# Kernel optimization log

Hardware: AMD Instinct MI355X
Metric: run time of the kernel (lower is better)

The kernel has to match this reference:

```python
import jax, jax.numpy as jnp
import numpy as np

B, T = 64, 64
H = 256
CLIP = 0.2


def _conv(x, W, b, s):
    y = jax.lax.conv_general_dilated(x, W, (s, s), 'VALID',
                                     dimension_numbers=('NHWC', 'HWIO', 'NHWC'))
    return jax.nn.leaky_relu(y + b, negative_slope=0.2)


def _lstm(x, Wk, Wr, b):
    # keras LSTM, gate order i,f,g,o; x: (B,T,256) -> (B,T,256)
    h0 = jnp.zeros((x.shape[0], H), x.dtype)

    def step(carry, xt):
        h, c = carry
        z = xt @ Wk + h @ Wr + b
        i, f, g, o = jnp.split(z, 4, axis=-1)
        c = jax.nn.sigmoid(f) * c + jax.nn.sigmoid(i) * jnp.tanh(g)
        h = jax.nn.sigmoid(o) * jnp.tanh(c)
        return (h, c), h

    _, hs = jax.lax.scan(step, (h0, h0), jnp.swapaxes(x, 0, 1))
    return jnp.swapaxes(hs, 0, 1)


def setup_inputs():
    key = jax.random.key(0)
    ks = jax.random.split(key, 24)
    s = 0.05
    x = jax.random.normal(ks[0], (B, T, 13, 8, 8), jnp.float32)
    a_taken = jax.random.randint(ks[1], (B, T), 0, 36)
    mask = jax.random.randint(ks[2], (B, T, 4096), 0, 2).astype(jnp.int32)
    # taken actions must be legal (mask=1), as in real rollouts
    bi = jnp.repeat(jnp.arange(B), T)
    ti = jnp.tile(jnp.arange(T), B)
    mask = mask.at[bi, ti, a_taken.reshape(-1)].set(1)
    lg_prob_old = -jnp.abs(jax.random.normal(ks[3], (B, T), jnp.float32)) - 1.0
    GAE = jax.random.normal(ks[4], (B, T), jnp.float32)
    old_v_pred = jax.random.normal(ks[5], (B, T), jnp.float32)
    returns = jax.random.normal(ks[6], (B, T), jnp.float32)
    return {
        'x': x, 'mask': mask, 'lg_prob_old': lg_prob_old, 'a_taken': a_taken,
        'GAE': GAE, 'old_v_pred': old_v_pred, 'returns': returns,
        'W1': jax.random.normal(ks[7], (2, 2, 8, 16), jnp.float32) * s,
        'b1': jnp.zeros((16,), jnp.float32),
        'W2': jax.random.normal(ks[8], (2, 2, 16, 32), jnp.float32) * s,
        'b2': jnp.zeros((32,), jnp.float32),
        'W3': jax.random.normal(ks[9], (2, 2, 32, 64), jnp.float32) * s,
        'b3': jnp.zeros((64,), jnp.float32),
        'W4': jax.random.normal(ks[10], (1, 1, 64, 128), jnp.float32) * s,
        'b4': jnp.zeros((128,), jnp.float32),
        'lstm_k': jax.random.normal(ks[11], (256, 1024), jnp.float32) * s,
        'lstm_r': jax.random.normal(ks[12], (256, 1024), jnp.float32) * s,
        'lstm_b': jnp.zeros((1024,), jnp.float32),
        'pir_W': jax.random.normal(ks[13], (256, 36), jnp.float32) * s,
        'pir_b': jnp.zeros((36,), jnp.float32),
        'pim_W': jax.random.normal(ks[14], (256, 4096), jnp.float32) * s,
        'pim_b': jnp.zeros((4096,), jnp.float32),
        'v_W': jax.random.normal(ks[15], (256, 1), jnp.float32) * s,
        'v_b': jnp.zeros((1,), jnp.float32),
    }


def reference(x, mask, lg_prob_old, a_taken, GAE, old_v_pred, returns,
              W1, b1, W2, b2, W3, b3, W4, b4,
              lstm_k, lstm_r, lstm_b, pir_W, pir_b, pim_W, pim_b, v_W, v_b):
    Bn, Tn = x.shape[0], x.shape[1]
    h = x.reshape(Bn * Tn, 13, 8, 8)  # NHWC: H=13, W=8, C=8
    h = _conv(h, W1, b1, 2)  # (BT,6,4,16)
    h = _conv(h, W2, b2, 1)  # (BT,5,3,32)
    h = _conv(h, W3, b3, 2)  # (BT,2,1,64)
    h = _conv(h, W4, b4, 1)  # (BT,2,1,128)
    # keras Flatten(data_format='channels_first') permutes dim1 to last then flattens
    h = jnp.transpose(h, (0, 2, 3, 1)).reshape(Bn, Tn, -1)  # (B,T,256)
    lstm = _lstm(h, lstm_k, lstm_r, lstm_b).reshape(-1, H)  # (BT,256)

    pir = jax.nn.softmax(lstm @ pir_W + pir_b, axis=-1)  # (BT,36)
    maskf = mask.reshape(-1, 4096).astype(jnp.float32)
    pim = jax.nn.softmax(lstm @ pim_W + pim_b, axis=-1) * maskf
    scale = jnp.sum(pim, axis=1, keepdims=True)
    pim = pim / jnp.where(scale > 0, scale, jnp.ones_like(scale))  # (BT,4096)
    vpred = lstm @ v_W + v_b  # (BT,1)

    lg_old = lg_prob_old.reshape(-1)
    a = a_taken.reshape(-1)
    gae = GAE.reshape(-1)
    ovp = old_v_pred.reshape(-1)
    ret = returns.reshape(-1)
    gae = (gae - jnp.mean(gae)) / (jnp.std(gae) + 1e-8)

    t = jnp.arange(a.shape[0])
    p = jnp.where(t % 2 == 0, pir[t, a], pim[t, a])  # alternating heads
    lg_new = jnp.log(p)
    rt = jnp.exp(lg_new - lg_old)
    pg1 = -gae * rt
    pg2 = -gae * jnp.clip(rt, 1.0 - CLIP, 1.0 + CLIP)
    pg_loss = jnp.mean(jnp.maximum(pg1, pg2))

    # faithful to original TF: (BT,1) vpred broadcast against (BT,) -> (BT,BT)
    vpredclipped = ovp + jnp.clip(vpred - ovp, -CLIP, CLIP)
    vf1 = jnp.square(vpred - ret)
    vf2 = jnp.square(vpredclipped - ret)
    vf_loss = 0.5 * jnp.mean(jnp.maximum(vf1, vf2))

    pim_e = pim + (1.0 - maskf)
    entropy = -jnp.sum(pir * jnp.log(pir)) - jnp.sum(pim_e * jnp.log(pim_e))
    loss = pg_loss - entropy + vf_loss
    return (loss, pg_loss, entropy, vf_loss)
```

## Files before the change

### kernel.cpp

```cpp
#include <hip/hip_runtime.h>

typedef unsigned short u16;
typedef unsigned int   u32;

#define BT   4096
#define TSEQ 64
#define NB   64

typedef __attribute__((ext_vector_type(8))) short  short8;
typedef __attribute__((ext_vector_type(4))) float  f32x4;
typedef __attribute__((ext_vector_type(2))) _Float16 h2;

__device__ __forceinline__ float bf(u16 v) {
    u32 u = ((u32)v) << 16;
    return __builtin_bit_cast(float, u);
}
__device__ __forceinline__ u16 f2b(float f) {
    u32 u = __builtin_bit_cast(u32, f);
    return (u16)((u + 0x7fffu + ((u >> 16) & 1u)) >> 16);
}
__device__ __forceinline__ float lrelu(float x) { return x > 0.f ? x : 0.2f * x; }
__device__ __forceinline__ h2 i2h(int v) { return __builtin_bit_cast(h2, v); }
__device__ __forceinline__ float dot2(int hbits, int wbits, float acc) {
#if __has_builtin(__builtin_amdgcn_fdot2)
    return __builtin_amdgcn_fdot2(i2h(hbits), i2h(wbits), acc, false);
#else
    h2 a = i2h(hbits), b = i2h(wbits);
    return acc + (float)a.x * (float)b.x + (float)a.y * (float)b.y;
#endif
}
__device__ __forceinline__ float fsigm(float x) { return 1.f / (1.f + __expf(-x)); }
__device__ __forceinline__ float ftanh(float x) { return 1.f - 2.f / (__expf(2.f * x) + 1.f); }
__device__ __forceinline__ float ldf(const void* p, int i, int f32) {
    return f32 ? ((const float*)p)[i] : bf(((const u16*)p)[i]);
}
__device__ __forceinline__ u16 ldb(const void* p, int i, int f32) {
    return f32 ? f2b(((const float*)p)[i]) : ((const u16*)p)[i];
}

struct PrepPtrs {
    const void *x, *W1, *b1, *W2, *b2, *W3, *b3, *W4, *b4;
    const void *Wr, *Wk, *Wpim, *Wpir, *Wv;
    const u16* probe;
    u16 *featbf, *PF, *PBk, *PBpim, *PBpir;
    float* scal; int* flag;
};

#define PACK_BLKS 776
#define CONV_BLKS 2048

__global__ __launch_bounds__(256) void prep_kernel(PrepPtrs P)
{
    const int bid = blockIdx.x, tid = threadIdx.x;
    const int lane = tid & 63;
    u16 pv = P.probe[2 * lane];
    int e = (pv >> 7) & 0xFF;
    unsigned long long m = __ballot(pv == 0 || (e >= 100 && e <= 130));
    const int f32 = (__popcll(m) < 48) ? 1 : 0;

    if (bid == 0 && tid < 32) { P.scal[tid] = 0.f; if (tid == 0) *P.flag = f32; }

    if (bid < PACK_BLKS) {
        u16 t8[8];
        if (bid < 128) {
            int gid = bid * 256 + tid;
            int col = gid & 1023, oct = gid >> 10;
#pragma unroll
            for (int j = 0; j < 8; j++) {
                float f = ldf(P.Wr, (oct * 8 + j) * 1024 + col, f32);
                _Float16 h = (_Float16)f;
                t8[j] = __builtin_bit_cast(unsigned short, h);
            }
            *(int4*)&P.PF[((size_t)oct * 1024 + col) * 8] = *(int4*)t8;
        } else if (bid < 256) {
            int gid = (bid - 128) * 256 + tid;
            int col = gid & 1023, oct = gid >> 10;
#pragma unroll
            for (int j = 0; j < 8; j++) t8[j] = ldb(P.Wk, (oct * 8 + j) * 1024 + col, f32);
            *(int4*)&P.PBk[((((size_t)(oct >> 2) << 10) + col) * 4 + (oct & 3)) * 8] = *(int4*)t8;
        } else if (bid < 768) {
            int gid = (bid - 256) * 256 + tid;
            int col = gid & 4095, oct = gid >> 12;
#pragma unroll
            for (int j = 0; j < 8; j++) t8[j] = ldb(P.Wpim, (size_t)(oct * 8 + j) * 4096 + col, f32);
            *(int4*)&P.PBpim[((((size_t)(oct >> 2) << 12) + col) * 4 + (oct & 3)) * 8] = *(int4*)t8;
        } else {
            int gid = (bid - 768) * 256 + tid;
            int col = gid & 63, oct = gid >> 6;
#pragma unroll
            for (int j = 0; j < 8; j++) {
                int k = oct * 8 + j;
                u16 v = 0;
                if (col < 36)       v = ldb(P.Wpir, k * 36 + col, f32);
                else if (col == 36) v = ldb(P.Wv, k, f32);
                t8[j] = v;
            }
            *(int4*)&P.PBpir[(((size_t)(oct >> 2) * 64 + col) * 4 + (oct & 3)) * 8] = *(int4*)t8;
        }
        return;
    }

    __shared__ __align__(16) u16 wl[19184];
    __shared__ float xs[2][832];
    __shared__ float c1[2][384];
    __shared__ float c2[2][480];
    __shared__ float c3[2][128];
    const int pair = bid - PACK_BLKS;
    const int sub = tid >> 7, stid = tid & 127;
    const int bt = pair * 2 + sub;

    {
        const void* sp[8] = {P.W1, P.b1, P.W2, P.b2, P.W3, P.b3, P.W4, P.b4};
        const int   sn[8] = {512, 16, 2048, 32, 8192, 64, 8192, 128};
        int o = 0;
        for (int s = 0; s < 8; s++) {
            for (int i = tid; i < sn[s]; i += 256) wl[o + i] = ldb(sp[s], i, f32);
            o += sn[s];
        }
    }
    for (int i = stid; i < 832; i += 128) xs[sub][i] = ldf(P.x, bt * 832 + i, f32);
    __syncthreads();

    for (int idx = stid; idx < 96; idx += 128) {
        int pos = idx >> 2, g = idx & 3;
        int oh = pos >> 2, ow = pos & 3;
        float a0 = bf(wl[512 + g * 4]), a1 = bf(wl[513 + g * 4]),
              a2 = bf(wl[514 + g * 4]), a3 = bf(wl[515 + g * 4]);
        for (int kh = 0; kh < 2; kh++)
            for (int kw = 0; kw < 2; kw++)
#pragma unroll
                for (int ic = 0; ic < 8; ic++) {
                    float xv = xs[sub][(2 * oh + kh) * 64 + (2 * ow + kw) * 8 + ic];
                    ushort4 w = *(const ushort4*)&wl[((kh * 2 + kw) * 8 + ic) * 16 + g * 4];
                    a0 += xv * bf(w.x); a1 += xv * bf(w.y);
                    a2 += xv * bf(w.z); a3 += xv * bf(w.w);
                }
        c1[sub][pos * 16 + g * 4]     = lrelu(a0);
        c1[sub][pos * 16 + g * 4 + 1] = lrelu(a1);
        c1[sub][pos * 16 + g * 4 + 2] = lrelu(a2);
        c1[sub][pos * 16 + g * 4 + 3] = lrelu(a3);
    }
    __syncthreads();

    for (int idx = stid; idx < 120; idx += 128) {
        int pos = idx >> 3, g = idx & 7;
        int oh = pos / 3, ow = pos % 3;
        float a0 = bf(wl[2576 + g * 4]), a1 = bf(wl[2577 + g * 4]),
              a2 = bf(wl[2578 + g * 4]), a3 = bf(wl[2579 + g * 4]);
        for (int kh = 0; kh < 2; kh++)
            for (int kw = 0; kw < 2; kw++)
#pragma unroll
                for (int ic = 0; ic < 16; ic++) {
                    float xv = c1[sub][((oh + kh) * 4 + (ow + kw)) * 16 + ic];
                    ushort4 w = *(const ushort4*)&wl[528 + ((kh * 2 + kw) * 16 + ic) * 32 + g * 4];
                    a0 += xv * bf(w.x); a1 += xv * bf(w.y);
                    a2 += xv * bf(w.z); a3 += xv * bf(w.w);
                }
        c2[sub][pos * 32 + g * 4]     = lrelu(a0);
        c2[sub][pos * 32 + g * 4 + 1] = lrelu(a1);
        c2[sub][pos * 32 + g * 4 + 2] = lrelu(a2);
        c2[sub][pos * 32 + g * 4 + 3] = lrelu(a3);
    }
    __syncthreads();

    for (int idx = stid; idx < 32; idx += 128) {
        int oh = idx >> 4, g = idx & 15;
        float a0 = bf(wl[10800 + g * 4]), a1 = bf(wl[10801 + g * 4]),
              a2 = bf(wl[10802 + g * 4]), a3 = bf(wl[10803 + g * 4]);
        for (int kh = 0; kh < 2; kh++)
            for (int kw = 0; kw < 2; kw++)
#pragma unroll
                for (int ic = 0; ic < 32; ic++) {
                    float xv = c2[sub][((2 * oh + kh) * 3 + kw) * 32 + ic];
                    ushort4 w = *(const ushort4*)&wl[2608 + ((kh * 2 + kw) * 32 + ic) * 64 + g * 4];
                    a0 += xv * bf(w.x); a1 += xv * bf(w.y);
                    a2 += xv * bf(w.z); a3 += xv * bf(w.w);
                }
        c3[sub][oh * 64 + g * 4]     = lrelu(a0);
        c3[sub][oh * 64 + g * 4 + 1] = lrelu(a1);
        c3[sub][oh * 64 + g * 4 + 2] = lrelu(a2);
        c3[sub][oh * 64 + g * 4 + 3] = lrelu(a3);
    }
    __syncthreads();

    for (int idx = stid; idx < 64; idx += 128) {
        int oh = idx >> 5, g = idx & 31;
        float a0 = bf(wl[19056 + g * 4]), a1 = bf(wl[19057 + g * 4]),
              a2 = bf(wl[19058 + g * 4]), a3 = bf(wl[19059 + g * 4]);
#pragma unroll
        for (int ic = 0; ic < 64; ic++) {
            float xv = c3[sub][oh * 64 + ic];
            ushort4 w = *(const ushort4*)&wl[10864 + ic * 128 + g * 4];
            a0 += xv * bf(w.x); a1 += xv * bf(w.y);
            a2 += xv * bf(w.z); a3 += xv * bf(w.w);
        }
        P.featbf[bt * 256 + (g * 4 + 0) * 2 + oh] = f2b(lrelu(a0));
        P.featbf[bt * 256 + (g * 4 + 1) * 2 + oh] = f2b(lrelu(a1));
        P.featbf[bt * 256 + (g * 4 + 2) * 2 + oh] = f2b(lrelu(a2));
        P.featbf[bt * 256 + (g * 4 + 3) * 2 + oh] = f2b(lrelu(a3));
    }
}

__global__ __launch_bounds__(256) void gemm_zx(
    const u16* __restrict__ Abf, const u16* __restrict__ PB,
    const void* __restrict__ bias, const int* __restrict__ flag,
    float* __restrict__ out)
{
    __shared__ __align__(16) u16 As[16 * 264];
    const int mb = blockIdx.y, nb = blockIdx.x, tid = threadIdx.x;
    const int f32 = *flag;
    const int m0 = mb * 16;
    {
        int row = tid >> 4, part = tid & 15;
        const f32x4* src = (const f32x4*)&Abf[(size_t)(m0 + row) * 256 + part * 16];
        f32x4 v0 = src[0], v1 = src[1];
        *(f32x4*)&As[row * 264 + part * 16] = v0;
        *(f32x4*)&As[row * 264 + part * 16 + 8] = v1;
    }
    __syncthreads();
    const int wv = tid >> 6, lane = tid & 63;
    const int colw = lane & 15, q = lane >> 4;
    const int n = nb * 64 + wv * 16 + colw;
    f32x4 acc = {0.f, 0.f, 0.f, 0.f};
#pragma unroll
    for (int kt = 0; kt < 8; kt++) {
        short8 a = *(const short8*)&As[colw * 264 + kt * 32 + q * 8];
        short8 b = *(const short8*)&PB[((((size_t)kt << 10) + n) * 4 + q) * 8];
        acc = __builtin_amdgcn_mfma_f32_16x16x32_bf16(a, b, acc, 0, 0, 0);
    }
    const float bj = ldf(bias, n, f32);
#pragma unroll
    for (int r = 0; r < 4; r++) {
        int row = q * 4 + r;
        out[(size_t)(m0 + row) * 1024 + n] = acc[r] + bj;
    }
}

#define NPRE 18
#define NLDS 7
#define NSTR (32 - NPRE - NLDS)
__global__ __launch_bounds__(1024)
__attribute__((amdgpu_waves_per_eu(4, 4)))
void lstm_kernel(
    const float* __restrict__ zx, const u16* __restrict__ PF,
    u16* __restrict__ hseqbf)
{
    __shared__ float zp[1024];
    __shared__ __align__(16) u16 h16[256];
    __shared__ u16 hist[TSEQ * 256];
    __shared__ __align__(16) int4 wlds[NLDS * 1024];
    const int b = blockIdx.x, tid = threadIdx.x;
    float c = 0.f;
    const int4* Pw = (const int4*)PF;

    int4 wr[NPRE];
#pragma unroll
    for (int j = 0; j < NPRE; j++) wr[j] = Pw[j * 1024 + tid];
#pragma unroll
    for (int j = 0; j < NLDS; j++) wlds[j * 1024 + tid] = Pw[(NPRE + j) * 1024 + tid];
    if (tid < 256) h16[tid] = 0;
    __syncthreads();

    for (int t = 0; t < TSEQ; t++) {
        int4 ws[NSTR];
#pragma unroll
        for (int j = 0; j < NSTR; j++) ws[j] = Pw[(NPRE + NLDS + j) * 1024 + tid];
        float zxv = zx[(size_t)(b * TSEQ + t) * 1024 + tid];

        float a0 = 0.f, a1 = 0.f, a2 = 0.f, a3 = 0.f;
#pragma unroll
        for (int j = 0; j < NPRE; j++) {
            int4 hv = *(const int4*)&h16[j * 8];
            a0 = dot2(hv.x, wr[j].x, a0);
            a1 = dot2(hv.y, wr[j].y, a1);
            a2 = dot2(hv.z, wr[j].z, a2);
            a3 = dot2(hv.w, wr[j].w, a3);
        }
#pragma unroll
        for (int j = 0; j < NLDS; j++) {
            int4 hv = *(const int4*)&h16[(NPRE + j) * 8];
            int4 w = wlds[j * 1024 + tid];
            a0 = dot2(hv.x, w.x, a0);
            a1 = dot2(hv.y, w.y, a1);
            a2 = dot2(hv.z, w.z, a2);
            a3 = dot2(hv.w, w.w, a3);
        }
#pragma unroll
        for (int j = 0; j < NSTR; j++) {
            int4 hv = *(const int4*)&h16[(NPRE + NLDS + j) * 8];
            a0 = dot2(hv.x, ws[j].x, a0);
            a1 = dot2(hv.y, ws[j].y, a1);
            a2 = dot2(hv.z, ws[j].z, a2);
            a3 = dot2(hv.w, ws[j].w, a3);
        }
        zp[tid] = ((a0 + a1) + (a2 + a3)) + zxv;
        __syncthreads();
        if (tid < 256) {
            float ai = zp[tid], af = zp[256 + tid], ag = zp[512 + tid], ao = zp[768 + tid];
            float ig = fsigm(ai), fg = fsigm(af), og = fsigm(ao);
            float gg = ftanh(ag);
            c = fg * c + ig * gg;
            float h = og * ftanh(c);
            h16[tid] = __builtin_bit_cast(unsigned short, (_Float16)h);
            hist[t * 256 + tid] = f2b(h);
        }
        __syncthreads();
    }
    for (int i = tid; i < TSEQ * 256; i += 1024)
        hseqbf[(size_t)b * (TSEQ * 256) + i] = hist[i];
}

__global__ __launch_bounds__(256) void pir_kernel(
    const u16* __restrict__ Abf, const u16* __restrict__ PB,
    const void* __restrict__ pir_b, const void* __restrict__ v_b,
    const int* __restrict__ flag, const int* __restrict__ a_taken,
    float* __restrict__ entpir, float* __restrict__ ppira, float* __restrict__ vpred)
{
    __shared__ __align__(16) u16 As[64 * 264];
    const int tid = threadIdx.x;
    const int wv = tid >> 6, lane = tid & 63;
    const int colw = lane & 15, q = lane >> 4;
    const int f32 = *flag;
    const int m0 = blockIdx.x * 64;

    for (int idx = tid; idx < 1024; idx += 256) {
        int row = idx >> 4, part = idx & 15;
        const f32x4* src = (const f32x4*)&Abf[(size_t)(m0 + row) * 256 + part * 16];
        f32x4 v0 = src[0], v1 = src[1];
        *(f32x4*)&As[row * 264 + part * 16] = v0;
        *(f32x4*)&As[row * 264 + part * 16 + 8] = v1;
    }
    __syncthreads();
    f32x4 acc[4];
#pragma unroll
    for (int nt = 0; nt < 4; nt++) acc[nt] = (f32x4){0.f, 0.f, 0.f, 0.f};
#pragma unroll
    for (int kt = 0; kt < 8; kt++) {
        short8 a = *(const short8*)&As[(wv * 16 + colw) * 264 + kt * 32 + q * 8];
#pragma unroll
        for (int nt = 0; nt < 4; nt++) {
            short8 b = *(const short8*)&PB[((((size_t)kt * 64) + nt * 16 + colw) * 4 + q) * 8];
            acc[nt] = __builtin_amdgcn_mfma_f32_16x16x32_bf16(a, b, acc[nt], 0, 0, 0);
        }
    }
    float* zq = (float*)&As[wv * 4224];
#pragma unroll
    for (int nt = 0; nt < 4; nt++) {
        int col = nt * 16 + colw;
        float bj = (col < 36) ? ldf(pir_b, col, f32)
                              : (col == 36 ? ldf(v_b, 0, f32) : 0.f);
#pragma unroll
        for (int r = 0; r < 4; r++)
            zq[(q * 4 + r) * 65 + col] = acc[nt][r] + bj;
    }
    if (lane < 16) {
        int R = m0 + wv * 16 + lane;
        const float* zrow = &zq[lane * 65];
        float Z = 0.f, U = 0.f;
        for (int cc = 0; cc < 36; cc++) {
            float z = zrow[cc];
            float ev = __expf(z);
            Z += ev; U += ev * z;
        }
        entpir[R] = logf(Z) - U / Z;
        ppira[R]  = __expf(zrow[a_taken[R]]) / Z;
        vpred[R]  = zrow[36];
    }
}

__global__ __launch_bounds__(256) void pim_kernel(
    const u16* __restrict__ Abf, const u16* __restrict__ PB,
    const void* __restrict__ pim_b, const int* __restrict__ flag,
    const int* __restrict__ mask, const int* __restrict__ a_taken,
    float* __restrict__ partS, float* __restrict__ partU, float* __restrict__ za)
{
    __shared__ __align__(16) u16 As[32 * 264];
    __shared__ float redS[4][32], redU[4][32];
    const int nb = blockIdx.x, mb = blockIdx.y, tid = threadIdx.x;
    const int wv = tid >> 6, lane = tid & 63;
    const int colw = lane & 15, q = lane >> 4;
    const int f32 = *flag;
    const int m0 = mb * 32;

    for (int idx = tid; idx < 512; idx += 256) {
        int row = idx >> 4, part = idx & 15;
        const f32x4* src = (const f32x4*)&Abf[(size_t)(m0 + row) * 256 + part * 16];
        f32x4 v0 = src[0], v1 = src[1];
        *(f32x4*)&As[row * 264 + part * 16] = v0;
        *(f32x4*)&As[row * 264 + part * 16 + 8] = v1;
    }
    __syncthreads();
    const int n = nb * 64 + wv * 16 + colw;
    f32x4 acc0 = {0.f, 0.f, 0.f, 0.f}, acc1 = {0.f, 0.f, 0.f, 0.f};
#pragma unroll
    for (int kt = 0; kt < 8; kt++) {
        short8 b = *(const short8*)&PB[((((size_t)kt << 12) + n) * 4 + q) * 8];
        short8 a0 = *(const short8*)&As[colw * 264 + kt * 32 + q * 8];
        short8 a1 = *(const short8*)&As[(16 + colw) * 264 + kt * 32 + q * 8];
        acc0 = __builtin_amdgcn_mfma_f32_16x16x32_bf16(a0, b, acc0, 0, 0, 0);
        acc1 = __builtin_amdgcn_mfma_f32_16x16x32_bf16(a1, b, acc1, 0, 0, 0);
    }
    const float bj = ldf(pim_b, n, f32);
#pragma unroll
    for (int half = 0; half < 2; half++) {
        const f32x4& acc = half ? acc1 : acc0;
        float sv[4], uv[4];
#pragma unroll
        for (int r = 0; r < 4; r++) {
            int row = m0 + half * 16 + q * 4 + r;
            float z = acc[r] + bj;
            int mm = mask[(size_t)row * 4096 + n];
            float ev = __expf(z);
            sv[r] = mm ? ev : 0.f;
            uv[r] = mm ? ev * z : 0.f;
            if (n == a_taken[row]) za[row] = z;
        }
#pragma unroll
        for (int r = 0; r < 4; r++) {
            for (int off = 1; off < 16; off <<= 1) {
                sv[r] += __shfl_xor(sv[r], off, 16);
                uv[r] += __shfl_xor(uv[r], off, 16);
            }
            if (colw == 0) {
                redS[wv][half * 16 + q * 4 + r] = sv[r];
                redU[wv][half * 16 + q * 4 + r] = uv[r];
            }
        }
    }
    __syncthreads();
    if (tid < 32) {
        float S = redS[0][tid] + redS[1][tid] + redS[2][tid] + redS[3][tid];
        float U = redU[0][tid] + redU[1][tid] + redU[2][tid] + redU[3][tid];
        partS[(size_t)(m0 + tid) * 64 + nb] = S;
        partU[(size_t)(m0 + tid) * 64 + nb] = U;
    }
}

#define TAIL_BLOCKS (16 + 256)
__global__ __launch_bounds__(256) void tail_kernel(
    const float* __restrict__ partS, const float* __restrict__ partU,
    const float* __restrict__ za,
    const float* __restrict__ entpir, const float* __restrict__ ppira,
    const float* __restrict__ vpred,
    const void* __restrict__ lgold, const void* __restrict__ gae,
    const void* __restrict__ ovp, const void* __restrict__ ret,
    float* __restrict__ scal, const int* __restrict__ flag,
    void* __restrict__ out)
{
    const int bid = blockIdx.x, tid = threadIdx.x;
    const int f32 = *flag;
    __shared__ float sh[8];
    __shared__ float mst[2];
    if (bid < 16) {
        const int r = bid * 256 + tid;
        float S = 0.f, U = 0.f;
#pragma unroll
        for (int t2 = 0; t2 < 64; t2++) {
            S += partS[(size_t)r * 64 + t2];
            U += partU[(size_t)r * 64 + t2];
        }
        float entpim = logf(S) - U / S;
        float ppima = __expf(za[r]) / S;
        float s = 0.f, s2 = 0.f;
        if (f32) {
            const float* gp = (const float*)gae;
            for (int i = tid; i < BT; i += 256) { float v = gp[i]; s += v; s2 += v * v; }
        } else {
            const u16* gp = (const u16*)gae;
            for (int i = tid; i < BT; i += 256) { float v = bf(gp[i]); s += v; s2 += v * v; }
        }
        for (int off = 32; off; off >>= 1) {
            s += __shfl_down(s, off, 64); s2 += __shfl_down(s2, off, 64);
        }
        if ((tid & 63) == 0) { sh[tid >> 6] = s; sh[4 + (tid >> 6)] = s2; }
        __syncthreads();
        if (tid == 0) {
            float Sa = sh[0] + sh[1] + sh[2] + sh[3];
            float S2a = sh[4] + sh[5] + sh[6] + sh[7];
            float mean = Sa / (float)BT;
            float var = S2a / (float)BT - mean * mean;
            mst[0] = mean; mst[1] = sqrtf(fmaxf(var, 0.f));
        }
        __syncthreads();
        float mean = mst[0], sd = mst[1];
        float p = (r & 1) ? ppima : ppira[r];
        float ln = logf(p);
        float rt = __expf(ln - ldf(lgold, r, f32));
        float g = (ldf(gae, r, f32) - mean) / (sd + 1e-8f);
        float rtc = fminf(fmaxf(rt, 0.8f), 1.2f);
        float pg = fmaxf(-g * rt, -g * rtc);
        float e12 = entpir[r] + entpim;
        for (int off = 32; off; off >>= 1) {
            pg += __shfl_down(pg, off, 64);
            e12 += __shfl_down(e12, off, 64);
        }
        if ((tid & 63) == 0) {
            atomicAdd(&scal[2], pg);
            atomicAdd(&scal[3], e12);
        }
    } else {
        const int i0 = (bid - 16) * 16;
        float s = 0.f;
        if (f32) {
            const float* rp = (const float*)ret;
            const float* op = (const float*)ovp;
            for (int rr = 0; rr < 16; rr++) {
                float vp = vpred[i0 + rr];
                for (int j = tid; j < BT; j += 256) {
                    float r2 = rp[j], o = op[j];
                    float d = fminf(fmaxf(vp - o, -0.2f), 0.2f);
                    float v1 = vp - r2;    v1 *= v1;
                    float v2 = o + d - r2; v2 *= v2;
                    s += fmaxf(v1, v2);
                }
            }
        } else {
            const u16* rp = (const u16*)ret;
            const u16* op = (const u16*)ovp;
            for (int rr = 0; rr < 16; rr++) {
                float vp = vpred[i0 + rr];
                for (int j = tid; j < BT; j += 256) {
                    float r2 = bf(rp[j]), o = bf(op[j]);
                    float d = fminf(fmaxf(vp - o, -0.2f), 0.2f);
                    float v1 = vp - r2;    v1 *= v1;
                    float v2 = o + d - r2; v2 *= v2;
                    s += fmaxf(v1, v2);
                }
            }
        }
        for (int off = 32; off; off >>= 1) s += __shfl_down(s, off, 64);
        if ((tid & 63) == 0) sh[tid >> 6] = s;
        __syncthreads();
        if (tid == 0) atomicAdd(&scal[5], sh[0] + sh[1] + sh[2] + sh[3]);
    }
    __threadfence();
    __syncthreads();
    if (tid == 0) {
        unsigned old = atomicAdd((unsigned int*)&scal[8], 1u);
        if (old == TAIL_BLOCKS - 1) {
            __threadfence();
            float pgs = atomicAdd(&scal[2], 0.f);
            float ents = atomicAdd(&scal[3], 0.f);
            float vfs = atomicAdd(&scal[5], 0.f);
            float pg = pgs / (float)BT;
            float vf = 0.5f * vfs / ((float)BT * (float)BT);
            float loss = pg - ents + vf;
            if (f32) {
                float* o = (float*)out;
                o[0] = loss; o[1] = pg; o[2] = ents; o[3] = vf;
            } else {
                u16* o = (u16*)out;
                o[0] = f2b(loss); o[1] = f2b(pg); o[2] = f2b(ents); o[3] = f2b(vf);
            }
        }
    }
}

extern "C" void kernel_launch(void* const* d_in, const int* in_sizes, int n_in,
                              void* d_out, int out_size, void* d_ws, size_t ws_size,
                              hipStream_t stream)
{
    const int* mask = (const int*)d_in[1];
    const int* a_tk = (const int*)d_in[3];

    float* p = (float*)d_ws;
    u16*   featbf = (u16*)p;            p += 524288;
    float* zx     = p;                  p += 4194304;
    u16*   hseqbf = (u16*)p;            p += 524288;
    u16*   PF     = (u16*)p;            p += 131072;
    u16*   PBk    = (u16*)p;            p += 131072;
    u16*   PBpim  = (u16*)p;            p += 524288;
    u16*   PBpir  = (u16*)p;            p += 8192;
    float* scal   = p;                  p += 32;
    int*   flag   = (int*)p;            p += 4;
    float* partS  = p;                  p += 262144;
    float* partU  = p;                  p += 262144;
    float* za     = p;                  p += 4096;
    float* entpir = p;                  p += 4096;
    float* ppira  = p;                  p += 4096;
    float* vpred  = p;                  p += 4096;

    PrepPtrs P;
    P.x = d_in[0];
    P.W1 = d_in[7];  P.b1 = d_in[8];
    P.W2 = d_in[9];  P.b2 = d_in[10];
    P.W3 = d_in[11]; P.b3 = d_in[12];
    P.W4 = d_in[13]; P.b4 = d_in[14];
    P.Wk = d_in[15]; P.Wr = d_in[16];
    P.Wpir = d_in[18]; P.Wpim = d_in[20]; P.Wv = d_in[22];
    P.probe = (const u16*)d_in[15];
    P.featbf = featbf; P.PF = PF; P.PBk = PBk; P.PBpim = PBpim; P.PBpir = PBpir;
    P.scal = scal; P.flag = flag;

    prep_kernel<<<PACK_BLKS + CONV_BLKS, 256, 0, stream>>>(P);
    gemm_zx<<<dim3(16, 256), 256, 0, stream>>>(featbf, PBk, d_in[17], flag, zx);
    lstm_kernel<<<NB, 1024, 0, stream>>>(zx, PF, hseqbf);
    pir_kernel<<<64, 256, 0, stream>>>(hseqbf, PBpir, d_in[19], d_in[23], flag,
                                       a_tk, entpir, ppira, vpred);
    pim_kernel<<<dim3(64, 128), 256, 0, stream>>>(hseqbf, PBpim, d_in[21], flag,
                                                  mask, a_tk, partS, partU, za);
    tail_kernel<<<TAIL_BLOCKS, 256, 0, stream>>>(
        partS, partU, za, entpir, ppira, vpred,
        d_in[2], d_in[4], d_in[5], d_in[6], scal, flag, (void*)d_out);
}
```

Baseline: 494.4 us.

## Split each LSTM sequence across four cooperating blocks with global-memory step sync

Each batch row's recurrence now runs on four blocks, each owning 64 hidden units across all four gates. The recurrent weights stay fully in registers (16 int4 per thread, K split in two halves) instead of being partly re-streamed from global memory every step. Blocks exchange their h slices through a double-buffered global array and an atomic counter with spin-waiting. The next step's zx is prefetched and h is written straight to global memory. This brings in cross-block synchronisation each timestep and relies on all 256 blocks being co-resident, which risks deadlock or added latency from the global round-trips.

```diff
diff --git a/kernel.cpp b/kernel.cpp
--- a/kernel.cpp
+++ b/kernel.cpp
@@ -43,7 +43,7 @@
     const void *Wr, *Wk, *Wpim, *Wpir, *Wv;
     const u16* probe;
     u16 *featbf, *PF, *PBk, *PBpim, *PBpir;
-    float* scal; int* flag;
+    float* scal; int* flag; int* fsync;
 };
 
 #define PACK_BLKS 776
@@ -58,7 +58,11 @@
     unsigned long long m = __ballot(pv == 0 || (e >= 100 && e <= 130));
     const int f32 = (__popcll(m) < 48) ? 1 : 0;
 
-    if (bid == 0 && tid < 32) { P.scal[tid] = 0.f; if (tid == 0) *P.flag = f32; }
+    if (bid == 0) {
+        if (tid < 32) P.scal[tid] = 0.f;
+        if (tid < 64) P.fsync[tid] = 0;
+        if (tid == 0) *P.flag = f32;
+    }
 
     if (bid < PACK_BLKS) {
         u16 t8[8];
@@ -236,78 +240,87 @@
     }
 }
 
-#define NPRE 18
-#define NLDS 7
-#define NSTR (32 - NPRE - NLDS)
-__global__ __launch_bounds__(1024)
-__attribute__((amdgpu_waves_per_eu(4, 4)))
-void lstm_kernel(
+__global__ __launch_bounds__(512) void lstm_kernel(
     const float* __restrict__ zx, const u16* __restrict__ PF,
-    u16* __restrict__ hseqbf)
+    u16* __restrict__ hseqbf, int* __restrict__ fsync,
+    unsigned int* __restrict__ hxg)
 {
-    __shared__ float zp[1024];
     __shared__ __align__(16) u16 h16[256];
-    __shared__ u16 hist[TSEQ * 256];
-    __shared__ __align__(16) int4 wlds[NLDS * 1024];
-    const int b = blockIdx.x, tid = threadIdx.x;
-    float c = 0.f;
+    __shared__ float zp[512];
+    const int bid = blockIdx.x;
+    const int b = bid & 63, p = bid >> 6;
+    const int tid = threadIdx.x;
+    const int c = tid & 255, khalf = tid >> 8;
+    const int gate = c >> 6, u6 = c & 63;
+    const int C = gate * 256 + p * 64 + u6;
     const int4* Pw = (const int4*)PF;
 
-    int4 wr[NPRE];
-#pragma unroll
-    for (int j = 0; j < NPRE; j++) wr[j] = Pw[j * 1024 + tid];
-#pragma unroll
-    for (int j = 0; j < NLDS; j++) wlds[j * 1024 + tid] = Pw[(NPRE + j) * 1024 + tid];
-    if (tid < 256) h16[tid] = 0;
-    __syncthreads();
-
+    int4 w[16];
+#pragma unroll
+    for (int j = 0; j < 16; j++) w[j] = Pw[(size_t)(khalf * 16 + j) * 1024 + C];
+
+    if (tid < 128) ((unsigned int*)h16)[tid] = 0u;
+    float cst = 0.f;
+    unsigned int* flagp = (unsigned int*)&fsync[b];
+    const size_t zrow0 = (size_t)b * TSEQ * 1024;
+    __syncthreads();
+
+    float zxv = (tid < 256) ? zx[zrow0 + C] : 0.f;
     for (int t = 0; t < TSEQ; t++) {
-        int4 ws[NSTR];
-#pragma unroll
-        for (int j = 0; j < NSTR; j++) ws[j] = Pw[(NPRE + NLDS + j) * 1024 + tid];
-        float zxv = zx[(size_t)(b * TSEQ + t) * 1024 + tid];
-
         float a0 = 0.f, a1 = 0.f, a2 = 0.f, a3 = 0.f;
 #pragma unroll
-        for (int j = 0; j < NPRE; j++) {
-            int4 hv = *(const int4*)&h16[j * 8];
-            a0 = dot2(hv.x, wr[j].x, a0);
-            a1 = dot2(hv.y, wr[j].y, a1);
-            a2 = dot2(hv.z, wr[j].z, a2);
-            a3 = dot2(hv.w, wr[j].w, a3);
-        }
-#pragma unroll
-        for (int j = 0; j < NLDS; j++) {
-            int4 hv = *(const int4*)&h16[(NPRE + j) * 8];
-            int4 w = wlds[j * 1024 + tid];
-            a0 = dot2(hv.x, w.x, a0);
-            a1 = dot2(hv.y, w.y, a1);
-            a2 = dot2(hv.z, w.z, a2);
-            a3 = dot2(hv.w, w.w, a3);
-        }
-#pragma unroll
-        for (int j = 0; j < NSTR; j++) {
-            int4 hv = *(const int4*)&h16[(NPRE + NLDS + j) * 8];
-            a0 = dot2(hv.x, ws[j].x, a0);
-            a1 = dot2(hv.y, ws[j].y, a1);
-            a2 = dot2(hv.z, ws[j].z, a2);
-            a3 = dot2(hv.w, ws[j].w, a3);
+        for (int j = 0; j < 16; j++) {
+            int4 hv = *(const int4*)&h16[(khalf * 16 + j) * 8];
+            a0 = dot2(hv.x, w[j].x, a0);
+            a1 = dot2(hv.y, w[j].y, a1);
+            a2 = dot2(hv.z, w[j].z, a2);
+            a3 = dot2(hv.w, w[j].w, a3);
         }
         zp[tid] = ((a0 + a1) + (a2 + a3)) + zxv;
         __syncthreads();
-        if (tid < 256) {
-            float ai = zp[tid], af = zp[256 + tid], ag = zp[512 + tid], ao = zp[768 + tid];
+
+        float zxn = 0.f;
+        if (tid < 256 && t + 1 < TSEQ) zxn = zx[zrow0 + (size_t)(t + 1) * 1024 + C];
+
+        if (tid < 64) {
+            float ai = zp[tid]       + zp[256 + tid];
+            float af = zp[64 + tid]  + zp[320 + tid];
+            float ag = zp[128 + tid] + zp[384 + tid];
+            float ao = zp[192 + tid] + zp[448 + tid];
             float ig = fsigm(ai), fg = fsigm(af), og = fsigm(ao);
             float gg = ftanh(ag);
-            c = fg * c + ig * gg;
-            float h = og * ftanh(c);
-            h16[tid] = __builtin_bit_cast(unsigned short, (_Float16)h);
-            hist[t * 256 + tid] = f2b(h);
+            cst = fg * cst + ig * gg;
+            float h = og * ftanh(cst);
+            u16 hb = __builtin_bit_cast(unsigned short, (_Float16)h);
+            hseqbf[(size_t)b * (TSEQ * 256) + t * 256 + p * 64 + tid] = f2b(h);
+            int hv_ = (int)hb;
+            int lo = __shfl(hv_, 2 * tid, 64);
+            int hi = __shfl(hv_, 2 * tid + 1, 64);
+            if (tid < 32) {
+                unsigned int dw = ((unsigned int)lo & 0xffffu) | ((unsigned int)hi << 16);
+                __hip_atomic_store(&hxg[(((b * 2 + (t & 1)) * 4 + p) * 32) + tid], dw,
+                                   __ATOMIC_RELAXED, __HIP_MEMORY_SCOPE_AGENT);
+            }
+            __threadfence();
+            if (tid == 0) {
+                __hip_atomic_fetch_add(flagp, 1u, __ATOMIC_RELEASE,
+                                       __HIP_MEMORY_SCOPE_AGENT);
+                const unsigned int tgt = 4u * (unsigned int)(t + 1);
+                while (__hip_atomic_load(flagp, __ATOMIC_ACQUIRE,
+                                         __HIP_MEMORY_SCOPE_AGENT) < tgt)
+                    __builtin_amdgcn_s_sleep(1);
+            }
         }
         __syncthreads();
-    }
-    for (int i = tid; i < TSEQ * 256; i += 1024)
-        hseqbf[(size_t)b * (TSEQ * 256) + i] = hist[i];
+        if (tid < 128) {
+            unsigned int dw = __hip_atomic_load(
+                &hxg[(size_t)((b * 2 + (t & 1)) * 4) * 32 + tid],
+                __ATOMIC_RELAXED, __HIP_MEMORY_SCOPE_AGENT);
+            ((unsigned int*)h16)[tid] = dw;
+        }
+        __syncthreads();
+        zxv = zxn;
+    }
 }
 
 __global__ __launch_bounds__(256) void pir_kernel(
@@ -579,6 +592,8 @@
     float* entpir = p;                  p += 4096;
     float* ppira  = p;                  p += 4096;
     float* vpred  = p;                  p += 4096;
+    int*   fsync  = (int*)p;            p += 64;
+    unsigned int* hxg = (unsigned int*)p; p += 16384;
 
     PrepPtrs P;
     P.x = d_in[0];
@@ -590,11 +605,11 @@
     P.Wpir = d_in[18]; P.Wpim = d_in[20]; P.Wv = d_in[22];
     P.probe = (const u16*)d_in[15];
     P.featbf = featbf; P.PF = PF; P.PBk = PBk; P.PBpim = PBpim; P.PBpir = PBpir;
-    P.scal = scal; P.flag = flag;
+    P.scal = scal; P.flag = flag; P.fsync = fsync;
 
     prep_kernel<<<PACK_BLKS + CONV_BLKS, 256, 0, stream>>>(P);
     gemm_zx<<<dim3(16, 256), 256, 0, stream>>>(featbf, PBk, d_in[17], flag, zx);
-    lstm_kernel<<<NB, 1024, 0, stream>>>(zx, PF, hseqbf);
+    lstm_kernel<<<256, 512, 0, stream>>>(zx, PF, hseqbf, fsync, hxg);
     pir_kernel<<<64, 256, 0, stream>>>(hseqbf, PBpir, d_in[19], d_in[23], flag,
                                        a_tk, entpir, ppira, vpred);
     pim_kernel<<<dim3(64, 128), 256, 0, stream>>>(hseqbf, PBpim, d_in[21], flag,
```

Result: slower. 1.050 ms (+112.3%).

## Restructure LSTM recurrence to one thread per hidden unit computing all four gates

Applied to the files above, without the earlier changes.

The recurrent kernel now runs 256 threads per batch row instead of 1024. Each thread computes all four gate pre-activations for its hidden unit, so the zp shared-memory exchange and the idle-thread gate phase go away. Recurrent weights are held mostly in registers (24 of 32 octets) with the rest in LDS, so nothing is re-streamed from global memory each step. The next step's input projection is prefetched, and h is written straight to global memory each step instead of being staged in a history buffer. The cost is 4x more serial dot-product work per thread and very high register pressure at one wave per EU, which may spill or lengthen each step's critical path.

```diff
diff --git a/kernel.cpp b/kernel.cpp
--- a/kernel.cpp
+++ b/kernel.cpp
@@ -236,78 +236,90 @@
     }
 }
 
-#define NPRE 18
-#define NLDS 7
-#define NSTR (32 - NPRE - NLDS)
-__global__ __launch_bounds__(1024)
-__attribute__((amdgpu_waves_per_eu(4, 4)))
+#define NOCT_REG 24
+#define NOCT_LDS 8
+__global__ __launch_bounds__(256)
+__attribute__((amdgpu_waves_per_eu(1, 1)))
 void lstm_kernel(
     const float* __restrict__ zx, const u16* __restrict__ PF,
     u16* __restrict__ hseqbf)
 {
-    __shared__ float zp[1024];
-    __shared__ __align__(16) u16 h16[256];
-    __shared__ u16 hist[TSEQ * 256];
-    __shared__ __align__(16) int4 wlds[NLDS * 1024];
-    const int b = blockIdx.x, tid = threadIdx.x;
-    float c = 0.f;
+    __shared__ __align__(16) u16 h16[264];
+    __shared__ __align__(16) int4 wlds[NOCT_LDS * 4 * 256];
+    const int b = blockIdx.x, u = threadIdx.x;
     const int4* Pw = (const int4*)PF;
 
-    int4 wr[NPRE];
-#pragma unroll
-    for (int j = 0; j < NPRE; j++) wr[j] = Pw[j * 1024 + tid];
-#pragma unroll
-    for (int j = 0; j < NLDS; j++) wlds[j * 1024 + tid] = Pw[(NPRE + j) * 1024 + tid];
-    if (tid < 256) h16[tid] = 0;
+    int4 wr[NOCT_REG][4];
+#pragma unroll
+    for (int o = 0; o < NOCT_REG; o++)
+#pragma unroll
+        for (int g = 0; g < 4; g++)
+            wr[o][g] = Pw[(size_t)o * 1024 + g * 256 + u];
+#pragma unroll
+    for (int o = 0; o < NOCT_LDS; o++)
+#pragma unroll
+        for (int g = 0; g < 4; g++)
+            wlds[(o * 4 + g) * 256 + u] = Pw[(size_t)(NOCT_REG + o) * 1024 + g * 256 + u];
+    if (u < 128) ((u32*)h16)[u] = 0u;
+    float cst = 0.f;
+    const size_t z0 = (size_t)b * TSEQ * 1024;
+    float zxv0 = zx[z0 + u], zxv1 = zx[z0 + 256 + u],
+          zxv2 = zx[z0 + 512 + u], zxv3 = zx[z0 + 768 + u];
     __syncthreads();
 
     for (int t = 0; t < TSEQ; t++) {
-        int4 ws[NSTR];
-#pragma unroll
-        for (int j = 0; j < NSTR; j++) ws[j] = Pw[(NPRE + NLDS + j) * 1024 + tid];
-        float zxv = zx[(size_t)(b * TSEQ + t) * 1024 + tid];
-
-        float a0 = 0.f, a1 = 0.f, a2 = 0.f, a3 = 0.f;
-#pragma unroll
-        for (int j = 0; j < NPRE; j++) {
-            int4 hv = *(const int4*)&h16[j * 8];
-            a0 = dot2(hv.x, wr[j].x, a0);
-            a1 = dot2(hv.y, wr[j].y, a1);
-            a2 = dot2(hv.z, wr[j].z, a2);
-            a3 = dot2(hv.w, wr[j].w, a3);
-        }
-#pragma unroll
-        for (int j = 0; j < NLDS; j++) {
-            int4 hv = *(const int4*)&h16[(NPRE + j) * 8];
-            int4 w = wlds[j * 1024 + tid];
-            a0 = dot2(hv.x, w.x, a0);
-            a1 = dot2(hv.y, w.y, a1);
-            a2 = dot2(hv.z, w.z, a2);
-            a3 = dot2(hv.w, w.w, a3);
-        }
-#pragma unroll
-        for (int j = 0; j < NSTR; j++) {
-            int4 hv = *(const int4*)&h16[(NPRE + NLDS + j) * 8];
-            a0 = dot2(hv.x, ws[j].x, a0);
-            a1 = dot2(hv.y, ws[j].y, a1);
-            a2 = dot2(hv.z, ws[j].z, a2);
-            a3 = dot2(hv.w, ws[j].w, a3);
-        }
-        zp[tid] = ((a0 + a1) + (a2 + a3)) + zxv;
+        float ax0 = 0.f, ay0 = 0.f, az0 = 0.f, aw0 = 0.f;
+        float ax1 = 0.f, ay1 = 0.f, az1 = 0.f, aw1 = 0.f;
+        float ax2 = 0.f, ay2 = 0.f, az2 = 0.f, aw2 = 0.f;
+        float ax3 = 0.f, ay3 = 0.f, az3 = 0.f, aw3 = 0.f;
+#pragma unroll
+        for (int o = 0; o < NOCT_REG; o++) {
+            int4 hv = *(const int4*)&h16[o * 8];
+            ax0 = dot2(hv.x, wr[o][0].x, ax0); ay0 = dot2(hv.y, wr[o][0].y, ay0);
+            az0 = dot2(hv.z, wr[o][0].z, az0); aw0 = dot2(hv.w, wr[o][0].w, aw0);
+            ax1 = dot2(hv.x, wr[o][1].x, ax1); ay1 = dot2(hv.y, wr[o][1].y, ay1);
+            az1 = dot2(hv.z, wr[o][1].z, az1); aw1 = dot2(hv.w, wr[o][1].w, aw1);
+            ax2 = dot2(hv.x, wr[o][2].x, ax2); ay2 = dot2(hv.y, wr[o][2].y, ay2);
+            az2 = dot2(hv.z, wr[o][2].z, az2); aw2 = dot2(hv.w, wr[o][2].w, aw2);
+            ax3 = dot2(hv.x, wr[o][3].x, ax3); ay3 = dot2(hv.y, wr[o][3].y, ay3);
+            az3 = dot2(hv.z, wr[o][3].z, az3); aw3 = dot2(hv.w, wr[o][3].w, aw3);
+        }
+#pragma unroll
+        for (int o = 0; o < NOCT_LDS; o++) {
+            int4 hv = *(const int4*)&h16[(NOCT_REG + o) * 8];
+            int4 w0 = wlds[(o * 4 + 0) * 256 + u];
+            int4 w1 = wlds[(o * 4 + 1) * 256 + u];
+            int4 w2 = wlds[(o * 4 + 2) * 256 + u];
+            int4 w3 = wlds[(o * 4 + 3) * 256 + u];
+            ax0 = dot2(hv.x, w0.x, ax0); ay0 = dot2(hv.y, w0.y, ay0);
+            az0 = dot2(hv.z, w0.z, az0); aw0 = dot2(hv.w, w0.w, aw0);
+            ax1 = dot2(hv.x, w1.x, ax1); ay1 = dot2(hv.y, w1.y, ay1);
+            az1 = dot2(hv.z, w1.z, az1); aw1 = dot2(hv.w, w1.w, aw1);
+            ax2 = dot2(hv.x, w2.x, ax2); ay2 = dot2(hv.y, w2.y, ay2);
+            az2 = dot2(hv.z, w2.z, az2); aw2 = dot2(hv.w, w2.w, aw2);
+            ax3 = dot2(hv.x, w3.x, ax3); ay3 = dot2(hv.y, w3.y, ay3);
+            az3 = dot2(hv.z, w3.z, az3); aw3 = dot2(hv.w, w3.w, aw3);
+        }
+        float zxn0 = 0.f, zxn1 = 0.f, zxn2 = 0.f, zxn3 = 0.f;
+        if (t + 1 < TSEQ) {
+            const size_t zr = z0 + (size_t)(t + 1) * 1024;
+            zxn0 = zx[zr + u]; zxn1 = zx[zr + 256 + u];
+            zxn2 = zx[zr + 512 + u]; zxn3 = zx[zr + 768 + u];
+        }
+        float zi = ((ax0 + ay0) + (az0 + aw0)) + zxv0;
+        float zf = ((ax1 + ay1) + (az1 + aw1)) + zxv1;
+        float zg = ((ax2 + ay2) + (az2 + aw2)) + zxv2;
+        float zo = ((ax3 + ay3) + (az3 + aw3)) + zxv3;
+        float ig = fsigm(zi), fg = fsigm(zf), og = fsigm(zo);
+        float gg = ftanh(zg);
+        cst = fg * cst + ig * gg;
+        float h = og * ftanh(cst);
         __syncthreads();
-        if (tid < 256) {
-            float ai = zp[tid], af = zp[256 + tid], ag = zp[512 + tid], ao = zp[768 + tid];
-            float ig = fsigm(ai), fg = fsigm(af), og = fsigm(ao);
-            float gg = ftanh(ag);
-            c = fg * c + ig * gg;
-            float h = og * ftanh(c);
-            h16[tid] = __builtin_bit_cast(unsigned short, (_Float16)h);
-            hist[t * 256 + tid] = f2b(h);
-        }
+        h16[u] = __builtin_bit_cast(unsigned short, (_Float16)h);
+        hseqbf[(size_t)b * (TSEQ * 256) + t * 256 + u] = f2b(h);
         __syncthreads();
-    }
-    for (int i = tid; i < TSEQ * 256; i += 1024)
-        hseqbf[(size_t)b * (TSEQ * 256) + i] = hist[i];
+        zxv0 = zxn0; zxv1 = zxn1; zxv2 = zxn2; zxv3 = zxn3;
+    }
 }
 
 __global__ __launch_bounds__(256) void pir_kernel(
@@ -594,7 +606,7 @@
 
     prep_kernel<<<PACK_BLKS + CONV_BLKS, 256, 0, stream>>>(P);
     gemm_zx<<<dim3(16, 256), 256, 0, stream>>>(featbf, PBk, d_in[17], flag, zx);
-    lstm_kernel<<<NB, 1024, 0, stream>>>(zx, PF, hseqbf);
+    lstm_kernel<<<NB, 256, 0, stream>>>(zx, PF, hseqbf);
     pir_kernel<<<64, 256, 0, stream>>>(hseqbf, PBpir, d_in[19], d_in[23], flag,
                                        a_tk, entpir, ppira, vpred);
     pim_kernel<<<dim3(64, 128), 256, 0, stream>>>(hseqbf, PBpim, d_in[21], flag,
```

Measured after the change: 805.1 us. +62.8%, slower.
